# Kernel optimization log

Hardware: AMD Instinct MI355X
Metric: run time of the kernel (lower is better)

The kernel has to match this reference:

```python
import jax, jax.numpy as jnp
import numpy as np

N = 1_000_000
RANK = 64
F_DIM = 64
DIMS_COARSE = 128
DIMS_FINE = 512


def setup_inputs() -> dict:
    key = jax.random.key(0)
    k1, k2, k3, k4, k5 = jax.random.split(key, 5)
    scale_u = (3.0 / RANK) ** (1.0 / 3.0)  # init_uncer_tensors scale
    lim = 1.0 / np.sqrt(RANK)  # torch Linear default init bound
    return {
        "xyz_sampled": jax.random.uniform(k1, (N, 3), dtype=jnp.float32),
        "line_coarse": 0.2 * jax.random.normal(k2, (3, RANK, DIMS_COARSE), dtype=jnp.float32),
        "line_fine": 0.2 * jax.random.normal(k3, (3, RANK, DIMS_FINE), dtype=jnp.float32),
        "uncert_lines": scale_u * jnp.ones((3, RANK, DIMS_COARSE), dtype=jnp.float32),
        "W_coarse": jax.random.uniform(k4, (F_DIM, RANK), minval=-lim, maxval=lim, dtype=jnp.float32),
        "W_fine": jax.random.uniform(k5, (F_DIM, RANK), minval=-lim, maxval=lim, dtype=jnp.float32),
    }


def _lerp1d(line, c):
    # line: (R, D) CP line coefficients; c: (N,) coord in [-1, 1]
    # equivalent to F.grid_sample(line[None,:,:,None], ..., align_corners=True)
    D = line.shape[-1]
    pos = (c + 1.0) * 0.5 * (D - 1)  # align_corners=True mapping
    i0 = jnp.clip(jnp.floor(pos).astype(jnp.int32), 0, D - 1)
    i1 = jnp.clip(i0 + 1, 0, D - 1)
    w = (pos - i0.astype(pos.dtype))[None, :]  # (1, N)
    return line[:, i0] * (1.0 - w) + line[:, i1] * w  # (R, N)


def _compute_feature(lines, xyz):
    # lines: (3, R, D); xyz: (N, 3) in [-1, 1] -> (N, R)
    p = _lerp1d(lines[0], xyz[:, 0])
    p = p * _lerp1d(lines[1], xyz[:, 1])
    p = p * _lerp1d(lines[2], xyz[:, 2])
    return p.T


def reference(xyz_sampled, line_coarse, line_fine, uncert_lines, W_coarse, W_fine):
    x = (xyz_sampled * 2.0 - 1.0).astype(jnp.float32)  # [0,1] -> [-1,1]
    coarse = _compute_feature(line_coarse, x) @ W_coarse.T  # (N, F_DIM)
    fine = _compute_feature(line_fine, x) @ W_fine.T        # (N, F_DIM)
    cat_feature = jnp.concatenate((coarse, fine), axis=-1)  # (N, 2*F_DIM)
    uncertainty = _compute_feature(uncert_lines, x).sum(-1)[:, None]  # (N, 1)
    return cat_feature, uncertainty
```

## Files before the change

### kernel.cpp

```cpp
#include <hip/hip_runtime.h>

#define N_PTS 1000000
#define RANK 64
#define DC 128
#define DF 512

typedef __attribute__((ext_vector_type(8))) short short8;
typedef __attribute__((ext_vector_type(4))) float f32x4;
typedef __attribute__((ext_vector_type(2))) float f32x2;

__device__ __forceinline__ unsigned short f2bf(float f) {
  unsigned int u = __float_as_uint(f);
  u += 0x7FFFu + ((u >> 16) & 1u);
  return (unsigned short)(u >> 16);
}

__device__ __forceinline__ float readlane_f(float v, int l) {
  return __uint_as_float(__builtin_amdgcn_readlane(__float_as_uint(v), l));
}

__global__ void build_pairs(const float* __restrict__ src, f32x2* __restrict__ dst, int D) {
  int tid = blockIdx.x * blockDim.x + threadIdx.x;
  if (tid >= 3 * D * RANK) return;
  int r = tid & (RANK - 1);
  int d = (tid >> 6) & (D - 1);
  int a = tid / (D * RANK);
  const float* s = src + (a * RANK + r) * D;
  int d1 = (d + 1 < D) ? d + 1 : D - 1;
  f32x2 v;
  v.x = s[d];
  v.y = s[d1];
  dst[tid] = v;
}

__global__ __launch_bounds__(256) void tensorcp_main(
    const float* __restrict__ xyz,
    const f32x2* __restrict__ CP,
    const f32x2* __restrict__ FP,
    const f32x2* __restrict__ UP,
    const float* __restrict__ Wc,
    const float* __restrict__ Wf,
    float* __restrict__ out)
{
  __shared__ __align__(16) unsigned short FcS[4][64][72];
  __shared__ __align__(16) unsigned short FfS[4][64][72];

  const int lane = threadIdx.x & 63;
  const int wv = threadIdx.x >> 6;
  const int batch = blockIdx.x * 4 + wv;
  if (batch * 64 >= N_PTS) return;
  const int p0 = batch * 64;

  const int fcol = lane & 15;
  const int kg = lane >> 4;

  const int myp = p0 + lane;
  const float px = xyz[myp * 3 + 0];
  const float py = xyz[myp * 3 + 1];
  const float pz = xyz[myp * 3 + 2];

  float pc0 = px * (float)(DC - 1), pc1 = py * (float)(DC - 1), pc2 = pz * (float)(DC - 1);
  float pf0 = px * (float)(DF - 1), pf1 = py * (float)(DF - 1), pf2 = pz * (float)(DF - 1);
  int ic0 = min(max((int)floorf(pc0), 0), DC - 1);
  int ic1 = min(max((int)floorf(pc1), 0), DC - 1);
  int ic2 = min(max((int)floorf(pc2), 0), DC - 1);
  int if0 = min(max((int)floorf(pf0), 0), DF - 1);
  int if1 = min(max((int)floorf(pf1), 0), DF - 1);
  int if2 = min(max((int)floorf(pf2), 0), DF - 1);
  float wc0 = pc0 - (float)ic0, wc1 = pc1 - (float)ic1, wc2 = pc2 - (float)ic2;
  float wf0 = pf0 - (float)if0, wf1 = pf1 - (float)if1, wf2 = pf2 - (float)if2;

  short8 Bc[8], Bf[8];
#pragma unroll
  for (int k = 0; k < 2; ++k) {
#pragma unroll
    for (int n = 0; n < 4; ++n) {
      const float* wp = Wc + (n * 16 + fcol) * 64 + k * 32 + kg * 8;
      f32x4 lo = *(const f32x4*)wp;
      f32x4 hi = *(const f32x4*)(wp + 4);
      short8 b;
      b[0] = (short)f2bf(lo[0]); b[1] = (short)f2bf(lo[1]);
      b[2] = (short)f2bf(lo[2]); b[3] = (short)f2bf(lo[3]);
      b[4] = (short)f2bf(hi[0]); b[5] = (short)f2bf(hi[1]);
      b[6] = (short)f2bf(hi[2]); b[7] = (short)f2bf(hi[3]);
      Bc[k * 4 + n] = b;
      const float* wp2 = Wf + (n * 16 + fcol) * 64 + k * 32 + kg * 8;
      f32x4 lo2 = *(const f32x4*)wp2;
      f32x4 hi2 = *(const f32x4*)(wp2 + 4);
      short8 b2;
      b2[0] = (short)f2bf(lo2[0]); b2[1] = (short)f2bf(lo2[1]);
      b2[2] = (short)f2bf(lo2[2]); b2[3] = (short)f2bf(lo2[3]);
      b2[4] = (short)f2bf(hi2[0]); b2[5] = (short)f2bf(hi2[1]);
      b2[6] = (short)f2bf(hi2[2]); b2[7] = (short)f2bf(hi2[3]);
      Bf[k * 4 + n] = b2;
    }
  }

  unsigned short (&myFc)[64][72] = FcS[wv];
  unsigned short (&myFf)[64][72] = FfS[wv];

  const f32x2* CPx = CP;
  const f32x2* CPy = CP + DC * RANK;
  const f32x2* CPz = CP + 2 * DC * RANK;
  const f32x2* FPx = FP;
  const f32x2* FPy = FP + DF * RANK;
  const f32x2* FPz = FP + 2 * DF * RANK;
  const f32x2* UPx = UP;
  const f32x2* UPy = UP + DC * RANK;
  const f32x2* UPz = UP + 2 * DC * RANK;

  float u_keep = 0.0f;

#pragma unroll 2
  for (int p = 0; p < 64; ++p) {
    const int s_ic0 = __builtin_amdgcn_readlane(ic0, p);
    const int s_ic1 = __builtin_amdgcn_readlane(ic1, p);
    const int s_ic2 = __builtin_amdgcn_readlane(ic2, p);
    const int s_if0 = __builtin_amdgcn_readlane(if0, p);
    const int s_if1 = __builtin_amdgcn_readlane(if1, p);
    const int s_if2 = __builtin_amdgcn_readlane(if2, p);
    const float s_wc0 = readlane_f(wc0, p);
    const float s_wc1 = readlane_f(wc1, p);
    const float s_wc2 = readlane_f(wc2, p);
    const float s_wf0 = readlane_f(wf0, p);
    const float s_wf1 = readlane_f(wf1, p);
    const float s_wf2 = readlane_f(wf2, p);

    const f32x2 c0 = CPx[s_ic0 * RANK + lane];
    const f32x2 c1 = CPy[s_ic1 * RANK + lane];
    const f32x2 c2 = CPz[s_ic2 * RANK + lane];
    const f32x2 g0 = FPx[s_if0 * RANK + lane];
    const f32x2 g1 = FPy[s_if1 * RANK + lane];
    const f32x2 g2 = FPz[s_if2 * RANK + lane];
    const f32x2 u0 = UPx[s_ic0 * RANK + lane];
    const f32x2 u1 = UPy[s_ic1 * RANK + lane];
    const f32x2 u2 = UPz[s_ic2 * RANK + lane];

    const float a0v = fmaf(s_wc0, c0.y - c0.x, c0.x);
    const float a1v = fmaf(s_wc1, c1.y - c1.x, c1.x);
    const float a2v = fmaf(s_wc2, c2.y - c2.x, c2.x);
    const float b0v = fmaf(s_wf0, g0.y - g0.x, g0.x);
    const float b1v = fmaf(s_wf1, g1.y - g1.x, g1.x);
    const float b2v = fmaf(s_wf2, g2.y - g2.x, g2.x);
    const float q0v = fmaf(s_wc0, u0.y - u0.x, u0.x);
    const float q1v = fmaf(s_wc1, u1.y - u1.x, u1.x);
    const float q2v = fmaf(s_wc2, u2.y - u2.x, u2.x);

    const float fc = a0v * a1v * a2v;
    const float ff = b0v * b1v * b2v;
    const float fu = q0v * q1v * q2v;

    myFc[p][lane] = f2bf(fc);
    myFf[p][lane] = f2bf(ff);

    float ssum = fu;
    ssum += __shfl_xor(ssum, 32, 64);
    ssum += __shfl_xor(ssum, 16, 64);
    ssum += __shfl_xor(ssum, 8, 64);
    ssum += __shfl_xor(ssum, 4, 64);
    ssum += __shfl_xor(ssum, 2, 64);
    ssum += __shfl_xor(ssum, 1, 64);
    if (lane == p) u_keep = ssum;
  }

  asm volatile("s_waitcnt lgkmcnt(0)" ::: "memory");

  const long long rowbase = (long long)p0 * 128;
#pragma unroll
  for (int m = 0; m < 4; ++m) {
    const int prow = m * 16 + fcol;
    const short8 a0 = *(const short8*)&myFc[prow][kg * 8];
    const short8 a1 = *(const short8*)&myFc[prow][32 + kg * 8];
    f32x4 accc[4];
#pragma unroll
    for (int n = 0; n < 4; ++n) {
      f32x4 z = {0.f, 0.f, 0.f, 0.f};
      z = __builtin_amdgcn_mfma_f32_16x16x32_bf16(a0, Bc[n], z, 0, 0, 0);
      z = __builtin_amdgcn_mfma_f32_16x16x32_bf16(a1, Bc[4 + n], z, 0, 0, 0);
      accc[n] = z;
    }
    const short8 e0 = *(const short8*)&myFf[prow][kg * 8];
    const short8 e1 = *(const short8*)&myFf[prow][32 + kg * 8];
    f32x4 accf[4];
#pragma unroll
    for (int n = 0; n < 4; ++n) {
      f32x4 z = {0.f, 0.f, 0.f, 0.f};
      z = __builtin_amdgcn_mfma_f32_16x16x32_bf16(e0, Bf[n], z, 0, 0, 0);
      z = __builtin_amdgcn_mfma_f32_16x16x32_bf16(e1, Bf[4 + n], z, 0, 0, 0);
      accf[n] = z;
    }
#pragma unroll
    for (int reg = 0; reg < 4; ++reg) {
      const long long ro = rowbase + (long long)(m * 16 + kg * 4 + reg) * 128;
#pragma unroll
      for (int n = 0; n < 4; ++n) {
        __builtin_nontemporal_store(accc[n][reg], &out[ro + n * 16 + fcol]);
        __builtin_nontemporal_store(accf[n][reg], &out[ro + 64 + n * 16 + fcol]);
      }
    }
  }

  __builtin_nontemporal_store(u_keep, &out[(long long)N_PTS * 128 + p0 + lane]);
}

extern "C" void kernel_launch(void* const* d_in, const int* in_sizes, int n_in,
                              void* d_out, int out_size, void* d_ws, size_t ws_size,
                              hipStream_t stream) {
  const float* xyz    = (const float*)d_in[0];
  const float* line_c = (const float*)d_in[1];
  const float* line_f = (const float*)d_in[2];
  const float* unc_l  = (const float*)d_in[3];
  const float* Wc     = (const float*)d_in[4];
  const float* Wf     = (const float*)d_in[5];
  float* out = (float*)d_out;

  f32x2* CP = (f32x2*)d_ws;
  f32x2* FP = CP + 3 * DC * RANK;
  f32x2* UP = FP + 3 * DF * RANK;

  const int tc = 3 * DC * RANK;
  const int tf = 3 * DF * RANK;
  build_pairs<<<(tc + 255) / 256, 256, 0, stream>>>(line_c, CP, DC);
  build_pairs<<<(tf + 255) / 256, 256, 0, stream>>>(line_f, FP, DF);
  build_pairs<<<(tc + 255) / 256, 256, 0, stream>>>(unc_l, UP, DC);

  const int nwaves = N_PTS / 64;
  const int nblocks = (nwaves + 3) / 4;
  tensorcp_main<<<nblocks, 256, 0, stream>>>(xyz, CP, FP, UP, Wc, Wf, out);
}
```

Baseline: 897.0 us.

## Split feature phases sequentially through one shared LDS buffer to raise occupancy

The single fused loop that computed coarse, fine and uncertainty features together becomes three sequential phases that share one per-wave LDS tile. Uncertainty is now reduced by staging bf16 values in LDS and summing 64 of them per lane, replacing the six-step shuffle reduction that ran every iteration. Coarse and fine GEMMs each run right after their own feature fill, and launch bounds now request 4 blocks per CU. The intent is to halve LDS use, lower register pressure and drop the per-point shuffles. In exchange, the uncertainty sum now goes through bf16 rounding, which loses precision, and the three phases serialize work the fused loop could overlap.

```diff
diff --git a/kernel.cpp b/kernel.cpp
--- a/kernel.cpp
+++ b/kernel.cpp
@@ -13,6 +13,10 @@
   unsigned int u = __float_as_uint(f);
   u += 0x7FFFu + ((u >> 16) & 1u);
   return (unsigned short)(u >> 16);
+}
+
+__device__ __forceinline__ float bf2f(unsigned short s) {
+  return __uint_as_float(((unsigned int)s) << 16);
 }
 
 __device__ __forceinline__ float readlane_f(float v, int l) {
@@ -33,7 +37,7 @@
   dst[tid] = v;
 }
 
-__global__ __launch_bounds__(256) void tensorcp_main(
+__global__ __launch_bounds__(256, 4) void tensorcp_main(
     const float* __restrict__ xyz,
     const f32x2* __restrict__ CP,
     const f32x2* __restrict__ FP,
@@ -42,8 +46,7 @@
     const float* __restrict__ Wf,
     float* __restrict__ out)
 {
-  __shared__ __align__(16) unsigned short FcS[4][64][72];
-  __shared__ __align__(16) unsigned short FfS[4][64][72];
+  __shared__ __align__(16) unsigned short FS[4][64][72];
 
   const int lane = threadIdx.x & 63;
   const int wv = threadIdx.x >> 6;
@@ -70,7 +73,63 @@
   float wc0 = pc0 - (float)ic0, wc1 = pc1 - (float)ic1, wc2 = pc2 - (float)ic2;
   float wf0 = pf0 - (float)if0, wf1 = pf1 - (float)if1, wf2 = pf2 - (float)if2;
 
-  short8 Bc[8], Bf[8];
+  unsigned short (&myF)[64][72] = FS[wv];
+
+  const f32x2* CPx = CP;
+  const f32x2* CPy = CP + DC * RANK;
+  const f32x2* CPz = CP + 2 * DC * RANK;
+  const f32x2* FPx = FP;
+  const f32x2* FPy = FP + DF * RANK;
+  const f32x2* FPz = FP + 2 * DF * RANK;
+  const f32x2* UPx = UP;
+  const f32x2* UPy = UP + DC * RANK;
+  const f32x2* UPz = UP + 2 * DC * RANK;
+
+#pragma unroll 4
+  for (int p = 0; p < 64; ++p) {
+    const int s_ic0 = __builtin_amdgcn_readlane(ic0, p);
+    const int s_ic1 = __builtin_amdgcn_readlane(ic1, p);
+    const int s_ic2 = __builtin_amdgcn_readlane(ic2, p);
+    const float s_wc0 = readlane_f(wc0, p);
+    const float s_wc1 = readlane_f(wc1, p);
+    const float s_wc2 = readlane_f(wc2, p);
+
+    const f32x2 u0 = UPx[s_ic0 * RANK + lane];
+    const f32x2 u1 = UPy[s_ic1 * RANK + lane];
+    const f32x2 u2 = UPz[s_ic2 * RANK + lane];
+    const float q0v = fmaf(s_wc0, u0.y - u0.x, u0.x);
+    const float q1v = fmaf(s_wc1, u1.y - u1.x, u1.x);
+    const float q2v = fmaf(s_wc2, u2.y - u2.x, u2.x);
+    myF[p][lane] = f2bf(q0v * q1v * q2v);
+  }
+  asm volatile("s_waitcnt lgkmcnt(0)" ::: "memory");
+  float usum = 0.0f;
+#pragma unroll
+  for (int j = 0; j < 8; ++j) {
+    short8 v = *(const short8*)&myF[lane][j * 8];
+#pragma unroll
+    for (int t = 0; t < 8; ++t) usum += bf2f((unsigned short)v[t]);
+  }
+  __builtin_nontemporal_store(usum, &out[(long long)N_PTS * 128 + p0 + lane]);
+
+#pragma unroll 4
+  for (int p = 0; p < 64; ++p) {
+    const int s_ic0 = __builtin_amdgcn_readlane(ic0, p);
+    const int s_ic1 = __builtin_amdgcn_readlane(ic1, p);
+    const int s_ic2 = __builtin_amdgcn_readlane(ic2, p);
+    const float s_wc0 = readlane_f(wc0, p);
+    const float s_wc1 = readlane_f(wc1, p);
+    const float s_wc2 = readlane_f(wc2, p);
+
+    const f32x2 c0 = CPx[s_ic0 * RANK + lane];
+    const f32x2 c1 = CPy[s_ic1 * RANK + lane];
+    const f32x2 c2 = CPz[s_ic2 * RANK + lane];
+    const float a0v = fmaf(s_wc0, c0.y - c0.x, c0.x);
+    const float a1v = fmaf(s_wc1, c1.y - c1.x, c1.x);
+    const float a2v = fmaf(s_wc2, c2.y - c2.x, c2.x);
+    myF[p][lane] = f2bf(a0v * a1v * a2v);
+  }
+  short8 Bc[8];
 #pragma unroll
   for (int k = 0; k < 2; ++k) {
 #pragma unroll
@@ -84,123 +143,80 @@
       b[4] = (short)f2bf(hi[0]); b[5] = (short)f2bf(hi[1]);
       b[6] = (short)f2bf(hi[2]); b[7] = (short)f2bf(hi[3]);
       Bc[k * 4 + n] = b;
-      const float* wp2 = Wf + (n * 16 + fcol) * 64 + k * 32 + kg * 8;
-      f32x4 lo2 = *(const f32x4*)wp2;
-      f32x4 hi2 = *(const f32x4*)(wp2 + 4);
-      short8 b2;
-      b2[0] = (short)f2bf(lo2[0]); b2[1] = (short)f2bf(lo2[1]);
-      b2[2] = (short)f2bf(lo2[2]); b2[3] = (short)f2bf(lo2[3]);
-      b2[4] = (short)f2bf(hi2[0]); b2[5] = (short)f2bf(hi2[1]);
-      b2[6] = (short)f2bf(hi2[2]); b2[7] = (short)f2bf(hi2[3]);
-      Bf[k * 4 + n] = b2;
-    }
-  }
-
-  unsigned short (&myFc)[64][72] = FcS[wv];
-  unsigned short (&myFf)[64][72] = FfS[wv];
-
-  const f32x2* CPx = CP;
-  const f32x2* CPy = CP + DC * RANK;
-  const f32x2* CPz = CP + 2 * DC * RANK;
-  const f32x2* FPx = FP;
-  const f32x2* FPy = FP + DF * RANK;
-  const f32x2* FPz = FP + 2 * DF * RANK;
-  const f32x2* UPx = UP;
-  const f32x2* UPy = UP + DC * RANK;
-  const f32x2* UPz = UP + 2 * DC * RANK;
-
-  float u_keep = 0.0f;
-
-#pragma unroll 2
+    }
+  }
+  asm volatile("s_waitcnt lgkmcnt(0)" ::: "memory");
+  const long long rowbase = (long long)p0 * 128;
+#pragma unroll
+  for (int m = 0; m < 4; ++m) {
+    const int prow = m * 16 + fcol;
+    const short8 a0 = *(const short8*)&myF[prow][kg * 8];
+    const short8 a1 = *(const short8*)&myF[prow][32 + kg * 8];
+#pragma unroll
+    for (int n = 0; n < 4; ++n) {
+      f32x4 z = {0.f, 0.f, 0.f, 0.f};
+      z = __builtin_amdgcn_mfma_f32_16x16x32_bf16(a0, Bc[n], z, 0, 0, 0);
+      z = __builtin_amdgcn_mfma_f32_16x16x32_bf16(a1, Bc[4 + n], z, 0, 0, 0);
+#pragma unroll
+      for (int reg = 0; reg < 4; ++reg) {
+        const long long ro = rowbase + (long long)(m * 16 + kg * 4 + reg) * 128;
+        __builtin_nontemporal_store(z[reg], &out[ro + n * 16 + fcol]);
+      }
+    }
+  }
+  asm volatile("s_waitcnt lgkmcnt(0)" ::: "memory");
+
+#pragma unroll 4
   for (int p = 0; p < 64; ++p) {
-    const int s_ic0 = __builtin_amdgcn_readlane(ic0, p);
-    const int s_ic1 = __builtin_amdgcn_readlane(ic1, p);
-    const int s_ic2 = __builtin_amdgcn_readlane(ic2, p);
     const int s_if0 = __builtin_amdgcn_readlane(if0, p);
     const int s_if1 = __builtin_amdgcn_readlane(if1, p);
     const int s_if2 = __builtin_amdgcn_readlane(if2, p);
-    const float s_wc0 = readlane_f(wc0, p);
-    const float s_wc1 = readlane_f(wc1, p);
-    const float s_wc2 = readlane_f(wc2, p);
     const float s_wf0 = readlane_f(wf0, p);
     const float s_wf1 = readlane_f(wf1, p);
     const float s_wf2 = readlane_f(wf2, p);
 
-    const f32x2 c0 = CPx[s_ic0 * RANK + lane];
-    const f32x2 c1 = CPy[s_ic1 * RANK + lane];
-    const f32x2 c2 = CPz[s_ic2 * RANK + lane];
     const f32x2 g0 = FPx[s_if0 * RANK + lane];
     const f32x2 g1 = FPy[s_if1 * RANK + lane];
     const f32x2 g2 = FPz[s_if2 * RANK + lane];
-    const f32x2 u0 = UPx[s_ic0 * RANK + lane];
-    const f32x2 u1 = UPy[s_ic1 * RANK + lane];
-    const f32x2 u2 = UPz[s_ic2 * RANK + lane];
-
-    const float a0v = fmaf(s_wc0, c0.y - c0.x, c0.x);
-    const float a1v = fmaf(s_wc1, c1.y - c1.x, c1.x);
-    const float a2v = fmaf(s_wc2, c2.y - c2.x, c2.x);
     const float b0v = fmaf(s_wf0, g0.y - g0.x, g0.x);
     const float b1v = fmaf(s_wf1, g1.y - g1.x, g1.x);
     const float b2v = fmaf(s_wf2, g2.y - g2.x, g2.x);
-    const float q0v = fmaf(s_wc0, u0.y - u0.x, u0.x);
-    const float q1v = fmaf(s_wc1, u1.y - u1.x, u1.x);
-    const float q2v = fmaf(s_wc2, u2.y - u2.x, u2.x);
-
-    const float fc = a0v * a1v * a2v;
-    const float ff = b0v * b1v * b2v;
-    const float fu = q0v * q1v * q2v;
-
-    myFc[p][lane] = f2bf(fc);
-    myFf[p][lane] = f2bf(ff);
-
-    float ssum = fu;
-    ssum += __shfl_xor(ssum, 32, 64);
-    ssum += __shfl_xor(ssum, 16, 64);
-    ssum += __shfl_xor(ssum, 8, 64);
-    ssum += __shfl_xor(ssum, 4, 64);
-    ssum += __shfl_xor(ssum, 2, 64);
-    ssum += __shfl_xor(ssum, 1, 64);
-    if (lane == p) u_keep = ssum;
-  }
-
-  asm volatile("s_waitcnt lgkmcnt(0)" ::: "memory");
-
-  const long long rowbase = (long long)p0 * 128;
+    myF[p][lane] = f2bf(b0v * b1v * b2v);
+  }
+  short8 Bf[8];
+#pragma unroll
+  for (int k = 0; k < 2; ++k) {
+#pragma unroll
+    for (int n = 0; n < 4; ++n) {
+      const float* wp = Wf + (n * 16 + fcol) * 64 + k * 32 + kg * 8;
+      f32x4 lo = *(const f32x4*)wp;
+      f32x4 hi = *(const f32x4*)(wp + 4);
+      short8 b;
+      b[0] = (short)f2bf(lo[0]); b[1] = (short)f2bf(lo[1]);
+      b[2] = (short)f2bf(lo[2]); b[3] = (short)f2bf(lo[3]);
+      b[4] = (short)f2bf(hi[0]); b[5] = (short)f2bf(hi[1]);
+      b[6] = (short)f2bf(hi[2]); b[7] = (short)f2bf(hi[3]);
+      Bf[k * 4 + n] = b;
+    }
+  }
+  asm volatile("s_waitcnt lgkmcnt(0)" ::: "memory");
 #pragma unroll
   for (int m = 0; m < 4; ++m) {
     const int prow = m * 16 + fcol;
-    const short8 a0 = *(const short8*)&myFc[prow][kg * 8];
-    const short8 a1 = *(const short8*)&myFc[prow][32 + kg * 8];
-    f32x4 accc[4];
+    const short8 a0 = *(const short8*)&myF[prow][kg * 8];
+    const short8 a1 = *(const short8*)&myF[prow][32 + kg * 8];
 #pragma unroll
     for (int n = 0; n < 4; ++n) {
       f32x4 z = {0.f, 0.f, 0.f, 0.f};
-      z = __builtin_amdgcn_mfma_f32_16x16x32_bf16(a0, Bc[n], z, 0, 0, 0);
-      z = __builtin_amdgcn_mfma_f32_16x16x32_bf16(a1, Bc[4 + n], z, 0, 0, 0);
-      accc[n] = z;
-    }
-    const short8 e0 = *(const short8*)&myFf[prow][kg * 8];
-    const short8 e1 = *(const short8*)&myFf[prow][32 + kg * 8];
-    f32x4 accf[4];
-#pragma unroll
-    for (int n = 0; n < 4; ++n) {
-      f32x4 z = {0.f, 0.f, 0.f, 0.f};
-      z = __builtin_amdgcn_mfma_f32_16x16x32_bf16(e0, Bf[n], z, 0, 0, 0);
-      z = __builtin_amdgcn_mfma_f32_16x16x32_bf16(e1, Bf[4 + n], z, 0, 0, 0);
-      accf[n] = z;
-    }
-#pragma unroll
-    for (int reg = 0; reg < 4; ++reg) {
-      const long long ro = rowbase + (long long)(m * 16 + kg * 4 + reg) * 128;
-#pragma unroll
-      for (int n = 0; n < 4; ++n) {
-        __builtin_nontemporal_store(accc[n][reg], &out[ro + n * 16 + fcol]);
-        __builtin_nontemporal_store(accf[n][reg], &out[ro + 64 + n * 16 + fcol]);
+      z = __builtin_amdgcn_mfma_f32_16x16x32_bf16(a0, Bf[n], z, 0, 0, 0);
+      z = __builtin_amdgcn_mfma_f32_16x16x32_bf16(a1, Bf[4 + n], z, 0, 0, 0);
+#pragma unroll
+      for (int reg = 0; reg < 4; ++reg) {
+        const long long ro = rowbase + (long long)(m * 16 + kg * 4 + reg) * 128;
+        __builtin_nontemporal_store(z[reg], &out[ro + 64 + n * 16 + fcol]);
       }
     }
   }
-
-  __builtin_nontemporal_store(u_keep, &out[(long long)N_PTS * 128 + p0 + lane]);
 }
 
 extern "C" void kernel_launch(void* const* d_in, const int* in_sizes, int n_in,
```

Result: faster. 831.1 us (-7.3%).
